# Kernel optimization log

Measured on AMD Instinct MI355X. Metric: run time of the kernel, lower is better.

## Reference

```python
import jax, jax.numpy as jnp
import numpy as np

N = 768           # atoms
C = 128           # channels (layer_dims = [128]*4)
A = 8             # atom types
RBF = 4
RBF_LOW, RBF_HIGH = 0.0, 2.5
EPS = 1e-12

# Levi-Civita tensor for the 1x1->1 tensor product
_E = np.zeros((3, 3, 3), np.float32)
_E[0, 1, 2] = _E[1, 2, 0] = _E[2, 0, 1] = 1.0
_E[0, 2, 1] = _E[2, 1, 0] = _E[1, 0, 2] = -1.0
EIJK = jnp.asarray(_E)


def setup_inputs() -> dict:
    key = jax.random.key(0)
    ks = jax.random.split(key, 16)
    r = jax.random.normal(ks[0], (N, 3), jnp.float32) * 2.0
    one_hot = jax.nn.one_hot(jax.random.randint(ks[1], (N,), 0, A), A, dtype=jnp.float32)

    def W(k, shape, fan_in):
        return jax.random.normal(k, shape, jnp.float32) / np.sqrt(fan_in).astype(np.float32)

    return dict(
        r=r, one_hot=one_hot,
        embed_W=W(ks[2], (C, A), A), embed_b=jnp.zeros((C,), jnp.float32),
        # 12 radial nets: layer0 uses ids 0-1, layer1 ids 2-6, layer2 ids 7-11
        Rw1=W(ks[3], (12, RBF, C), RBF), Rb1=jnp.zeros((12, C), jnp.float32),
        Rw2=W(ks[4], (12, C, C), C), Rb2=jnp.zeros((12, C), jnp.float32),
        si0_w0=W(ks[5], (C, C), C), si0_b0=jnp.zeros((C,), jnp.float32),
        si0_w1=W(ks[6], (C, C), C),
        si1_w0=W(ks[7], (C, 2 * C), 2 * C), si1_b0=jnp.zeros((C,), jnp.float32),
        si1_w1=W(ks[8], (C, 3 * C), 3 * C),
        si2_w0=W(ks[9], (C, 2 * C), 2 * C), si2_b0=jnp.zeros((C,), jnp.float32),
        si2_w1=W(ks[10], (C, 3 * C), 3 * C),
        nl_b0=jnp.zeros((C,), jnp.float32), nl_b1=jnp.zeros((C,), jnp.float32),
        pred_W=W(ks[11], (A, C), C), pred_b=jnp.zeros((A,), jnp.float32),
    )


def _gated(x, b):
    # norm-gated equivariant nonlinearity for l=1 features [N, C, 3]
    n = jnp.sqrt(jnp.maximum(jnp.sum(x * x, -1), EPS))
    return x * (jax.nn.elu(b[None, :] + n) / n)[..., None]


def reference(r, one_hot, embed_W, embed_b, Rw1, Rb1, Rw2, Rb2,
              si0_w0, si0_b0, si0_w1, si1_w0, si1_b0, si1_w1,
              si2_w0, si2_b0, si2_w1, nl_b0, nl_b1, pred_W, pred_b):
    rij = r[:, None, :] - r[None, :, :]                     # [N,N,3]
    dij = jnp.sqrt(jnp.maximum(jnp.sum(rij * rij, -1), EPS))  # [N,N]
    u = rij / (dij[..., None] + 1e-8)                        # unit vectors
    centers = jnp.linspace(RBF_LOW, RBF_HIGH, RBF)
    gamma = RBF / (RBF_HIGH - RBF_LOW)                       # 1 / spacing
    rbf = jnp.exp(-gamma * jnp.square(dij[..., None] - centers))  # [N,N,RBF]

    def radial(i):  # per-filter radial net on rbf features -> [N,N,C]
        h = jax.nn.relu(jnp.einsum('abr,rc->abc', rbf, Rw1[i]) + Rb1[i])
        return jnp.einsum('abc,cd->abd', h, Rw2[i]) + Rb2[i]

    def si(x, w, b=None):  # self-interaction linear over channel dim f
        y = jnp.einsum('afm,gf->agm', x, w)
        return y if b is None else y + b[:, None]

    e = (one_hot @ embed_W.T + embed_b)[..., None]           # [N,C,1]

    # layer 0: only an l=0 input exists
    c00 = jnp.einsum('abf,bfm->afm', radial(0), e)                 # 0x0->0
    c01 = jnp.einsum('abf,abi,bf->afi', radial(1), u, e[..., 0])   # 0x1->1
    x0 = jax.nn.elu(si(c00, si0_w0, si0_b0))
    x1 = _gated(si(c01, si0_w1), nl_b0)

    def full_layer(x0, x1, ri, w0, b0, w1):
        a0 = jnp.einsum('abf,bfm->afm', radial(ri), x0)                        # 0x0->0
        b1 = jnp.einsum('abf,abi,bf->afi', radial(ri + 1), u, x0[..., 0])      # 0x1->1
        a1 = jnp.einsum('abf,bfm->afm', radial(ri + 2), x1)                    # 1x0->1
        o0 = jnp.einsum('abf,abj,bfj->af', radial(ri + 3), u, x1)[..., None]   # 1x1->0
        o1 = jnp.einsum('ijk,abf,abj,bfk->afi', EIJK, radial(ri + 4), u, x1)   # 1x1->1
        y0 = si(jnp.concatenate([a0, o0], 1), w0, b0)   # [N,2C,1] -> [N,C,1]
        y1 = si(jnp.concatenate([b1, a1, o1], 1), w1)   # [N,3C,3] -> [N,C,3]
        return y0, y1

    x0, x1 = full_layer(x0, x1, 2, si1_w0, si1_b0, si1_w1)
    x0, x1 = jax.nn.elu(x0), _gated(x1, nl_b1)
    x0, x1 = full_layer(x0, x1, 7, si2_w0, si2_b0, si2_w1)  # last layer: no nonlinearity

    atom = (x0[..., 0] @ pred_W.T + pred_b)[..., None]      # [N,A,1]
    # (probability_scalars, missing_coordinates, atom_type_scalars)
    return x0, x1, atom
```

## Files before the change

### kernel.cpp

```cpp
#include <hip/hip_runtime.h>
#include <hip/hip_fp16.h>
#include <math.h>


constexpr int   N_    = 768;
constexpr int   C_    = 128;
constexpr int   M_    = 320;
constexpr float DMAX_ = 6.4f;
constexpr float GAMMA_ = 1.6f;

__global__ __launch_bounds__(256) void build_table_kernel(
    const float* __restrict__ Rw1, const float* __restrict__ Rb1,
    const float* __restrict__ Rw2, const float* __restrict__ Rb2,
    __half2* __restrict__ tab, float delta)
{
    const int f  = threadIdx.x & 127, fh = threadIdx.x >> 7;
    const int m0 = blockIdx.x * 4;

    __shared__ float hs[2][5][C_];

    float rbf[5][4];
    const float cent[4] = {0.0f, 2.5f / 3.0f, 5.0f / 3.0f, 2.5f};
#pragma unroll
    for (int mm = 0; mm < 5; ++mm) {
        int m = m0 + mm; if (m > M_ - 1) m = M_ - 1;
        const float d = (float)m * delta;
#pragma unroll
        for (int k = 0; k < 4; ++k) {
            const float t = d - cent[k];
            rbf[mm][k] = expf(-GAMMA_ * t * t);
        }
    }

    for (int ii = 0; ii < 6; ++ii) {
        const int i = fh * 6 + ii;
        float w1v[4];
#pragma unroll
        for (int k = 0; k < 4; ++k) w1v[k] = Rw1[(i * 4 + k) * C_ + f];
        const float b1v = Rb1[i * C_ + f];

        __syncthreads();
#pragma unroll
        for (int mm = 0; mm < 5; ++mm) {
            float acc = b1v;
#pragma unroll
            for (int k = 0; k < 4; ++k) acc = fmaf(rbf[mm][k], w1v[k], acc);
            hs[fh][mm][f] = fmaxf(acc, 0.0f);
        }
        __syncthreads();

        const float b2v = Rb2[i * C_ + f];
        float out[5] = {b2v, b2v, b2v, b2v, b2v};
        for (int c = 0; c < C_; ++c) {
            const float w = Rw2[(i * C_ + c) * C_ + f];
#pragma unroll
            for (int mm = 0; mm < 5; ++mm) out[mm] = fmaf(hs[fh][mm][c], w, out[mm]);
        }
#pragma unroll
        for (int mm = 0; mm < 4; ++mm) {
            const int m = m0 + mm;
            if (m < M_)
                tab[((size_t)m * 12 + i) * C_ + f] =
                    __floats2half2_rn(out[mm], out[mm + 1] - out[mm]);
        }
    }
}

__global__ __launch_bounds__(256) void embed_kernel(
    const float* __restrict__ onehot, const float* __restrict__ eW,
    const float* __restrict__ eb, float* __restrict__ e)
{
    const int idx = blockIdx.x * 256 + threadIdx.x;
    const int b = idx >> 7, f = idx & 127;
    float acc = eb[f];
#pragma unroll
    for (int t = 0; t < 8; ++t) acc = fmaf(onehot[b * 8 + t], eW[f * 8 + t], acc);
    e[idx] = acc;
}

template <int RI>
__device__ inline void pair_setup(const float* __restrict__ r, int a, int bbase,
                                  int tid, float4* pair, int* qoff)
{
    const float rax = r[a * 3 + 0], ray = r[a * 3 + 1], raz = r[a * 3 + 2];
    for (int i = tid; i < 384; i += 256) {
        const int b = bbase + i;
        const float dx = rax - r[b * 3 + 0];
        const float dy = ray - r[b * 3 + 1];
        const float dz = raz - r[b * 3 + 2];
        const float d2 = fmaf(dx, dx, fmaf(dy, dy, dz * dz));
        const float d  = sqrtf(fmaxf(d2, 1e-12f));
        const float inv = 1.0f / (d + 1e-8f);
        const float t = d * ((float)(M_ - 1) / DMAX_);
        int q = (int)t; q = q > M_ - 2 ? M_ - 2 : q;
        const float fr = fminf(t - (float)q, 1.0f);
        pair[i] = make_float4(dx * inv, dy * inv, dz * inv, fr);
        qoff[i] = (q * 12 + RI) * C_;
    }
}

__global__ __launch_bounds__(256, 8) void pair0_kernel(
    const float* __restrict__ r, const float* __restrict__ e,
    const __half2* __restrict__ tab, float* __restrict__ P)
{
    const int a = blockIdx.x >> 1, p = blockIdx.x & 1;
    const int tid = threadIdx.x;
    const int f = tid & 127, part = tid >> 7;
    const int bbase = p * 384;

    __shared__ float4 pair[384];
    __shared__ int    qoff[384];
    __shared__ float  sred[4][2][C_];

    pair_setup<0>(r, a, bbase, tid, pair, qoff);
    __syncthreads();

    float c00 = 0.f, cx = 0.f, cy = 0.f, cz = 0.f;
    const __half2* tabf = tab + f;
    const int iBeg = part * 192, iEnd = iBeg + 192;
    for (int i = iBeg; i < iEnd; ++i) {
        const float4 pr = pair[i];
        const __half2* tp = tabf + qoff[i];
        const __half2 h0 = tp[0], h1 = tp[C_];
        const float eb_ = e[(bbase + i) * C_ + f];
        const float fr = pr.w;
        const float2 v0 = __half22float2(h0);
        const float2 v1 = __half22float2(h1);
        const float t0 = fmaf(fr, v0.y, v0.x);
        const float t1 = fmaf(fr, v1.y, v1.x);
        c00 = fmaf(t0, eb_, c00);
        const float te = t1 * eb_;
        cx = fmaf(te, pr.x, cx); cy = fmaf(te, pr.y, cy); cz = fmaf(te, pr.z, cz);
    }

    sred[0][part][f] = c00;
    sred[1][part][f] = cx;
    sred[2][part][f] = cy;
    sred[3][part][f] = cz;
    __syncthreads();

    for (int idx = tid; idx < 4 * C_; idx += 256) {
        const int k = idx >> 7, c = idx & 127;
        P[((size_t)(p * N_ + a) * 4 + k) * C_ + c] =
            sred[k][0][c] + sred[k][1][c];
    }
}

template <int RI>
__global__ __launch_bounds__(256, 8) void pairF_kernel(
    const float* __restrict__ r, const uint2* __restrict__ xin,
    const __half2* __restrict__ tab, float* __restrict__ P)
{
    const int a = blockIdx.x >> 1, p = blockIdx.x & 1;
    const int tid = threadIdx.x;
    const int f = tid & 127, part = tid >> 7;
    const int bbase = p * 384;

    __shared__ float4 pair[384];
    __shared__ int    qoff[384];
    __shared__ float  sred[11][2][C_];

    pair_setup<RI>(r, a, bbase, tid, pair, qoff);
    __syncthreads();

    float a0 = 0.f, b1x = 0.f, b1y = 0.f, b1z = 0.f;
    float a1x = 0.f, a1y = 0.f, a1z = 0.f;
    float o0 = 0.f, o1x = 0.f, o1y = 0.f, o1z = 0.f;

    const __half2* tabf = tab + f;
    const uint2*   xf   = xin + (size_t)bbase * C_ + f;
    const int iBeg = part * 192, iEnd = iBeg + 192;
    for (int i = iBeg; i < iEnd; ++i) {
        const float4 pr = pair[i];
        const __half2* tp = tabf + qoff[i];
        const __half2 h0 = tp[0 * C_], h1 = tp[1 * C_], h2 = tp[2 * C_];
        const __half2 h3 = tp[3 * C_], h4 = tp[4 * C_];
        const uint2 xw = xf[(size_t)i * C_];

        const float fr = pr.w;
        const float2 v0 = __half22float2(h0);
        const float2 v1 = __half22float2(h1);
        const float2 v2 = __half22float2(h2);
        const float2 v3 = __half22float2(h3);
        const float2 v4 = __half22float2(h4);
        const float t0 = fmaf(fr, v0.y, v0.x);
        const float t1 = fmaf(fr, v1.y, v1.x);
        const float t2 = fmaf(fr, v2.y, v2.x);
        const float t3 = fmaf(fr, v3.y, v3.x);
        const float t4 = fmaf(fr, v4.y, v4.x);

        const float2 x01 = __half22float2(*(const __half2*)&xw.x);
        const float2 x23 = __half22float2(*(const __half2*)&xw.y);
        const float x0b = x01.x, xbx = x01.y, xby = x23.x, xbz = x23.y;

        a0 = fmaf(t0, x0b, a0);
        const float tb = t1 * x0b;
        b1x = fmaf(tb, pr.x, b1x); b1y = fmaf(tb, pr.y, b1y); b1z = fmaf(tb, pr.z, b1z);
        a1x = fmaf(t2, xbx, a1x); a1y = fmaf(t2, xby, a1y); a1z = fmaf(t2, xbz, a1z);
        const float ud = fmaf(pr.x, xbx, fmaf(pr.y, xby, pr.z * xbz));
        o0 = fmaf(t3, ud, o0);
        const float crx = pr.y * xbz - pr.z * xby;
        const float cry = pr.z * xbx - pr.x * xbz;
        const float crz = pr.x * xby - pr.y * xbx;
        o1x = fmaf(t4, crx, o1x); o1y = fmaf(t4, cry, o1y); o1z = fmaf(t4, crz, o1z);
    }

    sred[0][part][f] = a0;
    sred[1][part][f] = b1x; sred[2][part][f] = b1y; sred[3][part][f] = b1z;
    sred[4][part][f] = a1x; sred[5][part][f] = a1y; sred[6][part][f] = a1z;
    sred[7][part][f] = o0;
    sred[8][part][f] = o1x; sred[9][part][f] = o1y; sred[10][part][f] = o1z;
    __syncthreads();

    for (int idx = tid; idx < 11 * C_; idx += 256) {
        const int k = idx >> 7, c = idx & 127;
        P[((size_t)(p * N_ + a) * 11 + k) * C_ + c] =
            sred[k][0][c] + sred[k][1][c];
    }
}

__global__ __launch_bounds__(512) void finish0_kernel(
    const float* __restrict__ P,
    const float* __restrict__ w0, const float* __restrict__ b0v,
    const float* __restrict__ w1, const float* __restrict__ nlb,
    uint2* __restrict__ xout)
{
    const int a = blockIdx.x, tid = threadIdx.x;
    const int f = tid & 127;

    __shared__ float s[4 * C_];
    __shared__ float ys[4 * C_];

    for (int idx = tid; idx < 4 * C_; idx += 512)
        s[idx] = P[(size_t)a * 4 * C_ + idx] +
                 P[((size_t)(N_ + a) * 4) * C_ + idx];
    __syncthreads();

    {
        const int j = tid >> 7;
        float y;
        if (j == 0) {
            y = b0v[f];
            const float4* w = (const float4*)(w0 + (size_t)f * C_);
            for (int c4 = 0; c4 < C_ / 4; ++c4) {
                const float4 wv = w[c4];
                y = fmaf(wv.x, s[c4 * 4 + 0], y);
                y = fmaf(wv.y, s[c4 * 4 + 1], y);
                y = fmaf(wv.z, s[c4 * 4 + 2], y);
                y = fmaf(wv.w, s[c4 * 4 + 3], y);
            }
        } else {
            y = 0.f;
            const float4* w = (const float4*)(w1 + (size_t)f * C_);
            const float* sj = s + j * C_;
            for (int c4 = 0; c4 < C_ / 4; ++c4) {
                const float4 wv = w[c4];
                y = fmaf(wv.x, sj[c4 * 4 + 0], y);
                y = fmaf(wv.y, sj[c4 * 4 + 1], y);
                y = fmaf(wv.z, sj[c4 * 4 + 2], y);
                y = fmaf(wv.w, sj[c4 * 4 + 3], y);
            }
        }
        ys[j * C_ + f] = y;
    }
    __syncthreads();

    if (tid < C_) {
        const float y0 = ys[tid];
        const float yx = ys[C_ + tid], yy = ys[2 * C_ + tid], yz = ys[3 * C_ + tid];
        const float x0v = y0 > 0.f ? y0 : expm1f(y0);
        const float nsq = fmaf(yx, yx, fmaf(yy, yy, yz * yz));
        const float nn  = sqrtf(fmaxf(nsq, 1e-12f));
        const float g   = nlb[tid] + nn;
        const float sc  = (g > 0.f ? g : expm1f(g)) / nn;
        uint2 w;
        *(__half2*)&w.x = __floats2half2_rn(x0v, yx * sc);
        *(__half2*)&w.y = __floats2half2_rn(yy * sc, yz * sc);
        xout[(size_t)a * C_ + tid] = w;
    }
}

template <bool NONLIN, bool LAST>
__global__ __launch_bounds__(512) void finishF_kernel(
    const float* __restrict__ P,
    const float* __restrict__ w0, const float* __restrict__ b0v,
    const float* __restrict__ w1, const float* __restrict__ nlb,
    uint2* __restrict__ xout,
    float* __restrict__ out, const float* __restrict__ predW,
    const float* __restrict__ predb)
{
    const int a = blockIdx.x, tid = threadIdx.x;
    const int f = tid & 127;

    __shared__ float s[11 * C_];
    __shared__ float ys[4 * C_];

    for (int idx = tid; idx < 11 * C_; idx += 512)
        s[idx] = P[(size_t)a * 11 * C_ + idx] +
                 P[((size_t)(N_ + a) * 11) * C_ + idx];
    __syncthreads();

    {
        const int j = tid >> 7;
        float y;
        if (j == 0) {
            y = b0v[f];
            const float4* w = (const float4*)(w0 + (size_t)f * (2 * C_));
            const float* s0 = s + 0 * C_;
            const float* s7 = s + 7 * C_;
            for (int c4 = 0; c4 < C_ / 4; ++c4) {
                const float4 wa = w[c4];
                const float4 wb = w[C_ / 4 + c4];
                y = fmaf(wa.x, s0[c4 * 4 + 0], y);
                y = fmaf(wa.y, s0[c4 * 4 + 1], y);
                y = fmaf(wa.z, s0[c4 * 4 + 2], y);
                y = fmaf(wa.w, s0[c4 * 4 + 3], y);
                y = fmaf(wb.x, s7[c4 * 4 + 0], y);
                y = fmaf(wb.y, s7[c4 * 4 + 1], y);
                y = fmaf(wb.z, s7[c4 * 4 + 2], y);
                y = fmaf(wb.w, s7[c4 * 4 + 3], y);
            }
        } else {
            y = 0.f;
            const float4* w = (const float4*)(w1 + (size_t)f * (3 * C_));
            const float* sb = s + j * C_;
            const float* sa = s + (3 + j) * C_;
            const float* so = s + (7 + j) * C_;
            for (int c4 = 0; c4 < C_ / 4; ++c4) {
                const float4 w_b = w[c4];
                const float4 w_a = w[C_ / 4 + c4];
                const float4 w_o = w[2 * (C_ / 4) + c4];
                y = fmaf(w_b.x, sb[c4 * 4 + 0], y);
                y = fmaf(w_b.y, sb[c4 * 4 + 1], y);
                y = fmaf(w_b.z, sb[c4 * 4 + 2], y);
                y = fmaf(w_b.w, sb[c4 * 4 + 3], y);
                y = fmaf(w_a.x, sa[c4 * 4 + 0], y);
                y = fmaf(w_a.y, sa[c4 * 4 + 1], y);
                y = fmaf(w_a.z, sa[c4 * 4 + 2], y);
                y = fmaf(w_a.w, sa[c4 * 4 + 3], y);
                y = fmaf(w_o.x, so[c4 * 4 + 0], y);
                y = fmaf(w_o.y, so[c4 * 4 + 1], y);
                y = fmaf(w_o.z, so[c4 * 4 + 2], y);
                y = fmaf(w_o.w, so[c4 * 4 + 3], y);
            }
        }
        ys[j * C_ + f] = y;
    }
    __syncthreads();

    if (NONLIN) {
        if (tid < C_) {
            const float y0 = ys[tid];
            const float yx = ys[C_ + tid], yy = ys[2 * C_ + tid], yz = ys[3 * C_ + tid];
            const float x0v = y0 > 0.f ? y0 : expm1f(y0);
            const float nsq = fmaf(yx, yx, fmaf(yy, yy, yz * yz));
            const float nn  = sqrtf(fmaxf(nsq, 1e-12f));
            const float g   = nlb[tid] + nn;
            const float sc  = (g > 0.f ? g : expm1f(g)) / nn;
            uint2 w;
            *(__half2*)&w.x = __floats2half2_rn(x0v, yx * sc);
            *(__half2*)&w.y = __floats2half2_rn(yy * sc, yz * sc);
            xout[(size_t)a * C_ + tid] = w;
        }
    }
    if (LAST) {
        if (tid < C_) {
            const float y0 = ys[tid];
            const float yx = ys[C_ + tid], yy = ys[2 * C_ + tid], yz = ys[3 * C_ + tid];
            out[a * C_ + tid] = y0;
            float* o1 = out + N_ * C_;
            o1[a * (C_ * 3) + tid * 3 + 0] = yx;
            o1[a * (C_ * 3) + tid * 3 + 1] = yy;
            o1[a * (C_ * 3) + tid * 3 + 2] = yz;
        }
        __syncthreads();
        if (tid < 8) {
            float acc = predb[tid];
            for (int c = 0; c < C_; ++c)
                acc = fmaf(predW[tid * C_ + c], ys[c], acc);
            out[N_ * C_ + N_ * C_ * 3 + a * 8 + tid] = acc;
        }
    }
}

extern "C" void kernel_launch(void* const* d_in, const int* in_sizes, int n_in,
                              void* d_out, int out_size, void* d_ws, size_t ws_size,
                              hipStream_t stream)
{
    const float* r       = (const float*)d_in[0];
    const float* onehot  = (const float*)d_in[1];
    const float* embed_W = (const float*)d_in[2];
    const float* embed_b = (const float*)d_in[3];
    const float* Rw1     = (const float*)d_in[4];
    const float* Rb1     = (const float*)d_in[5];
    const float* Rw2     = (const float*)d_in[6];
    const float* Rb2     = (const float*)d_in[7];
    const float* si0_w0  = (const float*)d_in[8];
    const float* si0_b0  = (const float*)d_in[9];
    const float* si0_w1  = (const float*)d_in[10];
    const float* si1_w0  = (const float*)d_in[11];
    const float* si1_b0  = (const float*)d_in[12];
    const float* si1_w1  = (const float*)d_in[13];
    const float* si2_w0  = (const float*)d_in[14];
    const float* si2_b0  = (const float*)d_in[15];
    const float* si2_w1  = (const float*)d_in[16];
    const float* nl_b0   = (const float*)d_in[17];
    const float* nl_b1   = (const float*)d_in[18];
    const float* pred_W  = (const float*)d_in[19];
    const float* pred_b  = (const float*)d_in[20];
    (void)in_sizes; (void)n_in; (void)out_size; (void)ws_size;

    const float delta = DMAX_ / (float)(M_ - 1);

    char* wsb = (char*)d_ws;
    __half2* table = (__half2*)wsb;
    float*   e     = (float*)(wsb + 1966080);
    uint2*   xa    = (uint2*)(wsb + 1966080 + 393216);
    uint2*   xb    = (uint2*)(wsb + 1966080 + 393216 + 786432);
    float*   P     = (float*)(wsb + 1966080 + 393216 + 786432 * 2);

    float* out = (float*)d_out;

    build_table_kernel<<<M_ / 4, 256, 0, stream>>>(Rw1, Rb1, Rw2, Rb2, table, delta);
    embed_kernel<<<(N_ * C_) / 256, 256, 0, stream>>>(onehot, embed_W, embed_b, e);

    pair0_kernel<<<2 * N_, 256, 0, stream>>>(r, e, table, P);
    finish0_kernel<<<N_, 512, 0, stream>>>(P, si0_w0, si0_b0, si0_w1, nl_b0, xa);

    pairF_kernel<2><<<2 * N_, 256, 0, stream>>>(r, xa, table, P);
    finishF_kernel<true, false><<<N_, 512, 0, stream>>>(
        P, si1_w0, si1_b0, si1_w1, nl_b1, xb, nullptr, nullptr, nullptr);

    pairF_kernel<7><<<2 * N_, 256, 0, stream>>>(r, xb, table, P);
    finishF_kernel<false, true><<<N_, 512, 0, stream>>>(
        P, si2_w0, si2_b0, si2_w1, nullptr, nullptr, out, pred_W, pred_b);
}
```

Measured before the change: 537.5 us.

## Split pair work three ways, batch atoms in finish kernels, enlarge radial table

The pair kernels now split each atom's neighbours into three chunks instead of two, which launches more, smaller blocks and gives better occupancy. The finish kernels each handle three atoms per block, so every weight load is reused across three atoms, and they sum three partial buffers. The radial lookup table grows from 320 to 512 entries, which makes it more accurate but larger in cache. The RI template parameter becomes a runtime argument, and the half-to-float conversions are rewritten. The extra partial sums add global traffic in the finish stage, and the fewer finish blocks (256) may leave the GPU underfilled.

```diff
diff --git a/kernel.cpp b/kernel.cpp
--- a/kernel.cpp
+++ b/kernel.cpp
@@ -3,11 +3,18 @@
 #include <math.h>
 
 
-constexpr int   N_    = 768;
-constexpr int   C_    = 128;
-constexpr int   M_    = 320;
-constexpr float DMAX_ = 6.4f;
+constexpr int   N_     = 768;
+constexpr int   C_     = 128;
+constexpr int   M_     = 512;
+constexpr int   NSPLIT = 3;
+constexpr int   NB_    = N_ / NSPLIT;
+constexpr int   TA_    = 3;
+constexpr float DMAX_  = 6.4f;
 constexpr float GAMMA_ = 1.6f;
+
+__device__ inline float lerp_vd(float fr, __half2 vd) {
+    return fmaf(fr, __half2float(__high2half(vd)), __half2float(__low2half(vd)));
+}
 
 __global__ __launch_bounds__(256) void build_table_kernel(
     const float* __restrict__ Rw1, const float* __restrict__ Rb1,
@@ -78,12 +85,11 @@
     e[idx] = acc;
 }
 
-template <int RI>
 __device__ inline void pair_setup(const float* __restrict__ r, int a, int bbase,
-                                  int tid, float4* pair, int* qoff)
+                                  int tid, int RI, float4* pair, int* qoff)
 {
     const float rax = r[a * 3 + 0], ray = r[a * 3 + 1], raz = r[a * 3 + 2];
-    for (int i = tid; i < 384; i += 256) {
+    for (int i = tid; i < NB_; i += 256) {
         const int b = bbase + i;
         const float dx = rax - r[b * 3 + 0];
         const float dy = ray - r[b * 3 + 1];
@@ -103,31 +109,30 @@
     const float* __restrict__ r, const float* __restrict__ e,
     const __half2* __restrict__ tab, float* __restrict__ P)
 {
-    const int a = blockIdx.x >> 1, p = blockIdx.x & 1;
+    const int a = blockIdx.x / NSPLIT, p = blockIdx.x - a * NSPLIT;
     const int tid = threadIdx.x;
     const int f = tid & 127, part = tid >> 7;
-    const int bbase = p * 384;
-
-    __shared__ float4 pair[384];
-    __shared__ int    qoff[384];
+    const int bbase = p * NB_;
+
+    __shared__ float4 pair[NB_];
+    __shared__ int    qoff[NB_];
     __shared__ float  sred[4][2][C_];
 
-    pair_setup<0>(r, a, bbase, tid, pair, qoff);
+    pair_setup(r, a, bbase, tid, 0, pair, qoff);
     __syncthreads();
 
     float c00 = 0.f, cx = 0.f, cy = 0.f, cz = 0.f;
     const __half2* tabf = tab + f;
-    const int iBeg = part * 192, iEnd = iBeg + 192;
+    const float*   ef   = e + (size_t)bbase * C_ + f;
+    const int iBeg = part * (NB_ / 2), iEnd = iBeg + (NB_ / 2);
     for (int i = iBeg; i < iEnd; ++i) {
         const float4 pr = pair[i];
         const __half2* tp = tabf + qoff[i];
         const __half2 h0 = tp[0], h1 = tp[C_];
-        const float eb_ = e[(bbase + i) * C_ + f];
+        const float eb_ = ef[(size_t)i * C_];
         const float fr = pr.w;
-        const float2 v0 = __half22float2(h0);
-        const float2 v1 = __half22float2(h1);
-        const float t0 = fmaf(fr, v0.y, v0.x);
-        const float t1 = fmaf(fr, v1.y, v1.x);
+        const float t0 = lerp_vd(fr, h0);
+        const float t1 = lerp_vd(fr, h1);
         c00 = fmaf(t0, eb_, c00);
         const float te = t1 * eb_;
         cx = fmaf(te, pr.x, cx); cy = fmaf(te, pr.y, cy); cz = fmaf(te, pr.z, cz);
@@ -141,26 +146,24 @@
 
     for (int idx = tid; idx < 4 * C_; idx += 256) {
         const int k = idx >> 7, c = idx & 127;
-        P[((size_t)(p * N_ + a) * 4 + k) * C_ + c] =
-            sred[k][0][c] + sred[k][1][c];
-    }
-}
-
-template <int RI>
+        P[((size_t)(p * N_ + a) * 4) * C_ + idx] = sred[k][0][c] + sred[k][1][c];
+    }
+}
+
 __global__ __launch_bounds__(256, 8) void pairF_kernel(
     const float* __restrict__ r, const uint2* __restrict__ xin,
-    const __half2* __restrict__ tab, float* __restrict__ P)
-{
-    const int a = blockIdx.x >> 1, p = blockIdx.x & 1;
+    const __half2* __restrict__ tab, int RI, float* __restrict__ P)
+{
+    const int a = blockIdx.x / NSPLIT, p = blockIdx.x - a * NSPLIT;
     const int tid = threadIdx.x;
     const int f = tid & 127, part = tid >> 7;
-    const int bbase = p * 384;
-
-    __shared__ float4 pair[384];
-    __shared__ int    qoff[384];
+    const int bbase = p * NB_;
+
+    __shared__ float4 pair[NB_];
+    __shared__ int    qoff[NB_];
     __shared__ float  sred[11][2][C_];
 
-    pair_setup<RI>(r, a, bbase, tid, pair, qoff);
+    pair_setup(r, a, bbase, tid, RI, pair, qoff);
     __syncthreads();
 
     float a0 = 0.f, b1x = 0.f, b1y = 0.f, b1z = 0.f;
@@ -169,7 +172,7 @@
 
     const __half2* tabf = tab + f;
     const uint2*   xf   = xin + (size_t)bbase * C_ + f;
-    const int iBeg = part * 192, iEnd = iBeg + 192;
+    const int iBeg = part * (NB_ / 2), iEnd = iBeg + (NB_ / 2);
     for (int i = iBeg; i < iEnd; ++i) {
         const float4 pr = pair[i];
         const __half2* tp = tabf + qoff[i];
@@ -178,20 +181,18 @@
         const uint2 xw = xf[(size_t)i * C_];
 
         const float fr = pr.w;
-        const float2 v0 = __half22float2(h0);
-        const float2 v1 = __half22float2(h1);
-        const float2 v2 = __half22float2(h2);
-        const float2 v3 = __half22float2(h3);
-        const float2 v4 = __half22float2(h4);
-        const float t0 = fmaf(fr, v0.y, v0.x);
-        const float t1 = fmaf(fr, v1.y, v1.x);
-        const float t2 = fmaf(fr, v2.y, v2.x);
-        const float t3 = fmaf(fr, v3.y, v3.x);
-        const float t4 = fmaf(fr, v4.y, v4.x);
-
-        const float2 x01 = __half22float2(*(const __half2*)&xw.x);
-        const float2 x23 = __half22float2(*(const __half2*)&xw.y);
-        const float x0b = x01.x, xbx = x01.y, xby = x23.x, xbz = x23.y;
+        const float t0 = lerp_vd(fr, h0);
+        const float t1 = lerp_vd(fr, h1);
+        const float t2 = lerp_vd(fr, h2);
+        const float t3 = lerp_vd(fr, h3);
+        const float t4 = lerp_vd(fr, h4);
+
+        const __half2 xh01 = *(const __half2*)&xw.x;
+        const __half2 xh23 = *(const __half2*)&xw.y;
+        const float x0b = __half2float(__low2half(xh01));
+        const float xbx = __half2float(__high2half(xh01));
+        const float xby = __half2float(__low2half(xh23));
+        const float xbz = __half2float(__high2half(xh23));
 
         a0 = fmaf(t0, x0b, a0);
         const float tb = t1 * x0b;
@@ -214,8 +215,7 @@
 
     for (int idx = tid; idx < 11 * C_; idx += 256) {
         const int k = idx >> 7, c = idx & 127;
-        P[((size_t)(p * N_ + a) * 11 + k) * C_ + c] =
-            sred[k][0][c] + sred[k][1][c];
+        P[((size_t)(p * N_ + a) * 11) * C_ + idx] = sred[k][0][c] + sred[k][1][c];
     }
 }
 
@@ -225,58 +225,71 @@
     const float* __restrict__ w1, const float* __restrict__ nlb,
     uint2* __restrict__ xout)
 {
-    const int a = blockIdx.x, tid = threadIdx.x;
-    const int f = tid & 127;
-
-    __shared__ float s[4 * C_];
-    __shared__ float ys[4 * C_];
-
-    for (int idx = tid; idx < 4 * C_; idx += 512)
-        s[idx] = P[(size_t)a * 4 * C_ + idx] +
-                 P[((size_t)(N_ + a) * 4) * C_ + idx];
-    __syncthreads();
-
-    {
-        const int j = tid >> 7;
-        float y;
-        if (j == 0) {
-            y = b0v[f];
-            const float4* w = (const float4*)(w0 + (size_t)f * C_);
-            for (int c4 = 0; c4 < C_ / 4; ++c4) {
-                const float4 wv = w[c4];
-                y = fmaf(wv.x, s[c4 * 4 + 0], y);
-                y = fmaf(wv.y, s[c4 * 4 + 1], y);
-                y = fmaf(wv.z, s[c4 * 4 + 2], y);
-                y = fmaf(wv.w, s[c4 * 4 + 3], y);
+    const int a0_ = blockIdx.x * TA_, tid = threadIdx.x;
+    const int f = tid & 127, j = tid >> 7;
+
+    __shared__ float s[TA_][4 * C_];
+    __shared__ float ys[TA_][4 * C_];
+
+    for (int t = 0; t < TA_; ++t)
+        for (int idx = tid; idx < 4 * C_; idx += 512) {
+            float acc = 0.f;
+            for (int sp = 0; sp < NSPLIT; ++sp)
+                acc += P[((size_t)(sp * N_ + a0_ + t) * 4) * C_ + idx];
+            s[t][idx] = acc;
+        }
+    __syncthreads();
+
+    float acc[TA_];
+    if (j == 0) {
+        const float b0 = b0v[f];
+#pragma unroll
+        for (int t = 0; t < TA_; ++t) acc[t] = b0;
+        const float4* w = (const float4*)(w0 + (size_t)f * C_);
+        for (int c4 = 0; c4 < C_ / 4; ++c4) {
+            const float4 wv = w[c4];
+#pragma unroll
+            for (int t = 0; t < TA_; ++t) {
+                const float4 sv = *(const float4*)&s[t][c4 * 4];
+                acc[t] = fmaf(wv.x, sv.x, acc[t]);
+                acc[t] = fmaf(wv.y, sv.y, acc[t]);
+                acc[t] = fmaf(wv.z, sv.z, acc[t]);
+                acc[t] = fmaf(wv.w, sv.w, acc[t]);
             }
-        } else {
-            y = 0.f;
-            const float4* w = (const float4*)(w1 + (size_t)f * C_);
-            const float* sj = s + j * C_;
-            for (int c4 = 0; c4 < C_ / 4; ++c4) {
-                const float4 wv = w[c4];
-                y = fmaf(wv.x, sj[c4 * 4 + 0], y);
-                y = fmaf(wv.y, sj[c4 * 4 + 1], y);
-                y = fmaf(wv.z, sj[c4 * 4 + 2], y);
-                y = fmaf(wv.w, sj[c4 * 4 + 3], y);
+        }
+    } else {
+#pragma unroll
+        for (int t = 0; t < TA_; ++t) acc[t] = 0.f;
+        const float4* w = (const float4*)(w1 + (size_t)f * C_);
+        for (int c4 = 0; c4 < C_ / 4; ++c4) {
+            const float4 wv = w[c4];
+#pragma unroll
+            for (int t = 0; t < TA_; ++t) {
+                const float4 sv = *(const float4*)&s[t][j * C_ + c4 * 4];
+                acc[t] = fmaf(wv.x, sv.x, acc[t]);
+                acc[t] = fmaf(wv.y, sv.y, acc[t]);
+                acc[t] = fmaf(wv.z, sv.z, acc[t]);
+                acc[t] = fmaf(wv.w, sv.w, acc[t]);
             }
         }
-        ys[j * C_ + f] = y;
-    }
-    __syncthreads();
-
-    if (tid < C_) {
-        const float y0 = ys[tid];
-        const float yx = ys[C_ + tid], yy = ys[2 * C_ + tid], yz = ys[3 * C_ + tid];
+    }
+#pragma unroll
+    for (int t = 0; t < TA_; ++t) ys[t][j * C_ + f] = acc[t];
+    __syncthreads();
+
+    if (tid < TA_ * C_) {
+        const int t = tid >> 7, ff = tid & 127;
+        const float y0 = ys[t][ff];
+        const float yx = ys[t][C_ + ff], yy = ys[t][2 * C_ + ff], yz = ys[t][3 * C_ + ff];
         const float x0v = y0 > 0.f ? y0 : expm1f(y0);
         const float nsq = fmaf(yx, yx, fmaf(yy, yy, yz * yz));
         const float nn  = sqrtf(fmaxf(nsq, 1e-12f));
-        const float g   = nlb[tid] + nn;
+        const float g   = nlb[ff] + nn;
         const float sc  = (g > 0.f ? g : expm1f(g)) / nn;
         uint2 w;
         *(__half2*)&w.x = __floats2half2_rn(x0v, yx * sc);
         *(__half2*)&w.y = __floats2half2_rn(yy * sc, yz * sc);
-        xout[(size_t)a * C_ + tid] = w;
+        xout[(size_t)(a0_ + t) * C_ + ff] = w;
     }
 }
 
@@ -289,96 +302,110 @@
     float* __restrict__ out, const float* __restrict__ predW,
     const float* __restrict__ predb)
 {
-    const int a = blockIdx.x, tid = threadIdx.x;
-    const int f = tid & 127;
-
-    __shared__ float s[11 * C_];
-    __shared__ float ys[4 * C_];
-
-    for (int idx = tid; idx < 11 * C_; idx += 512)
-        s[idx] = P[(size_t)a * 11 * C_ + idx] +
-                 P[((size_t)(N_ + a) * 11) * C_ + idx];
-    __syncthreads();
-
-    {
-        const int j = tid >> 7;
-        float y;
-        if (j == 0) {
-            y = b0v[f];
-            const float4* w = (const float4*)(w0 + (size_t)f * (2 * C_));
-            const float* s0 = s + 0 * C_;
-            const float* s7 = s + 7 * C_;
-            for (int c4 = 0; c4 < C_ / 4; ++c4) {
-                const float4 wa = w[c4];
-                const float4 wb = w[C_ / 4 + c4];
-                y = fmaf(wa.x, s0[c4 * 4 + 0], y);
-                y = fmaf(wa.y, s0[c4 * 4 + 1], y);
-                y = fmaf(wa.z, s0[c4 * 4 + 2], y);
-                y = fmaf(wa.w, s0[c4 * 4 + 3], y);
-                y = fmaf(wb.x, s7[c4 * 4 + 0], y);
-                y = fmaf(wb.y, s7[c4 * 4 + 1], y);
-                y = fmaf(wb.z, s7[c4 * 4 + 2], y);
-                y = fmaf(wb.w, s7[c4 * 4 + 3], y);
+    const int a0_ = blockIdx.x * TA_, tid = threadIdx.x;
+    const int f = tid & 127, j = tid >> 7;
+
+    __shared__ float s[TA_][11 * C_];
+    __shared__ float ys[TA_][4 * C_];
+
+    for (int t = 0; t < TA_; ++t)
+        for (int idx = tid; idx < 11 * C_; idx += 512) {
+            float acc = 0.f;
+            for (int sp = 0; sp < NSPLIT; ++sp)
+                acc += P[((size_t)(sp * N_ + a0_ + t) * 11) * C_ + idx];
+            s[t][idx] = acc;
+        }
+    __syncthreads();
+
+    float acc[TA_];
+    if (j == 0) {
+        const float b0 = b0v[f];
+#pragma unroll
+        for (int t = 0; t < TA_; ++t) acc[t] = b0;
+        const float4* w = (const float4*)(w0 + (size_t)f * (2 * C_));
+        for (int c4 = 0; c4 < C_ / 4; ++c4) {
+            const float4 wa = w[c4];
+            const float4 wb = w[C_ / 4 + c4];
+#pragma unroll
+            for (int t = 0; t < TA_; ++t) {
+                const float4 s0 = *(const float4*)&s[t][c4 * 4];
+                const float4 s7 = *(const float4*)&s[t][7 * C_ + c4 * 4];
+                acc[t] = fmaf(wa.x, s0.x, acc[t]);
+                acc[t] = fmaf(wa.y, s0.y, acc[t]);
+                acc[t] = fmaf(wa.z, s0.z, acc[t]);
+                acc[t] = fmaf(wa.w, s0.w, acc[t]);
+                acc[t] = fmaf(wb.x, s7.x, acc[t]);
+                acc[t] = fmaf(wb.y, s7.y, acc[t]);
+                acc[t] = fmaf(wb.z, s7.z, acc[t]);
+                acc[t] = fmaf(wb.w, s7.w, acc[t]);
             }
-        } else {
-            y = 0.f;
-            const float4* w = (const float4*)(w1 + (size_t)f * (3 * C_));
-            const float* sb = s + j * C_;
-            const float* sa = s + (3 + j) * C_;
-            const float* so = s + (7 + j) * C_;
-            for (int c4 = 0; c4 < C_ / 4; ++c4) {
-                const float4 w_b = w[c4];
-                const float4 w_a = w[C_ / 4 + c4];
-                const float4 w_o = w[2 * (C_ / 4) + c4];
-                y = fmaf(w_b.x, sb[c4 * 4 + 0], y);
-                y = fmaf(w_b.y, sb[c4 * 4 + 1], y);
-                y = fmaf(w_b.z, sb[c4 * 4 + 2], y);
-                y = fmaf(w_b.w, sb[c4 * 4 + 3], y);
-                y = fmaf(w_a.x, sa[c4 * 4 + 0], y);
-                y = fmaf(w_a.y, sa[c4 * 4 + 1], y);
-                y = fmaf(w_a.z, sa[c4 * 4 + 2], y);
-                y = fmaf(w_a.w, sa[c4 * 4 + 3], y);
-                y = fmaf(w_o.x, so[c4 * 4 + 0], y);
-                y = fmaf(w_o.y, so[c4 * 4 + 1], y);
-                y = fmaf(w_o.z, so[c4 * 4 + 2], y);
-                y = fmaf(w_o.w, so[c4 * 4 + 3], y);
+        }
+    } else {
+#pragma unroll
+        for (int t = 0; t < TA_; ++t) acc[t] = 0.f;
+        const float4* w = (const float4*)(w1 + (size_t)f * (3 * C_));
+        for (int c4 = 0; c4 < C_ / 4; ++c4) {
+            const float4 wb = w[c4];
+            const float4 wa = w[C_ / 4 + c4];
+            const float4 wo = w[2 * (C_ / 4) + c4];
+#pragma unroll
+            for (int t = 0; t < TA_; ++t) {
+                const float4 sb = *(const float4*)&s[t][j * C_ + c4 * 4];
+                const float4 sa = *(const float4*)&s[t][(3 + j) * C_ + c4 * 4];
+                const float4 so = *(const float4*)&s[t][(7 + j) * C_ + c4 * 4];
+                acc[t] = fmaf(wb.x, sb.x, acc[t]);
+                acc[t] = fmaf(wb.y, sb.y, acc[t]);
+                acc[t] = fmaf(wb.z, sb.z, acc[t]);
+                acc[t] = fmaf(wb.w, sb.w, acc[t]);
+                acc[t] = fmaf(wa.x, sa.x, acc[t]);
+                acc[t] = fmaf(wa.y, sa.y, acc[t]);
+                acc[t] = fmaf(wa.z, sa.z, acc[t]);
+                acc[t] = fmaf(wa.w, sa.w, acc[t]);
+                acc[t] = fmaf(wo.x, so.x, acc[t]);
+                acc[t] = fmaf(wo.y, so.y, acc[t]);
+                acc[t] = fmaf(wo.z, so.z, acc[t]);
+                acc[t] = fmaf(wo.w, so.w, acc[t]);
             }
         }
-        ys[j * C_ + f] = y;
-    }
+    }
+#pragma unroll
+    for (int t = 0; t < TA_; ++t) ys[t][j * C_ + f] = acc[t];
     __syncthreads();
 
     if (NONLIN) {
-        if (tid < C_) {
-            const float y0 = ys[tid];
-            const float yx = ys[C_ + tid], yy = ys[2 * C_ + tid], yz = ys[3 * C_ + tid];
+        if (tid < TA_ * C_) {
+            const int t = tid >> 7, ff = tid & 127;
+            const float y0 = ys[t][ff];
+            const float yx = ys[t][C_ + ff], yy = ys[t][2 * C_ + ff], yz = ys[t][3 * C_ + ff];
             const float x0v = y0 > 0.f ? y0 : expm1f(y0);
             const float nsq = fmaf(yx, yx, fmaf(yy, yy, yz * yz));
             const float nn  = sqrtf(fmaxf(nsq, 1e-12f));
-            const float g   = nlb[tid] + nn;
+            const float g   = nlb[ff] + nn;
             const float sc  = (g > 0.f ? g : expm1f(g)) / nn;
             uint2 w;
             *(__half2*)&w.x = __floats2half2_rn(x0v, yx * sc);
             *(__half2*)&w.y = __floats2half2_rn(yy * sc, yz * sc);
-            xout[(size_t)a * C_ + tid] = w;
+            xout[(size_t)(a0_ + t) * C_ + ff] = w;
         }
     }
     if (LAST) {
-        if (tid < C_) {
-            const float y0 = ys[tid];
-            const float yx = ys[C_ + tid], yy = ys[2 * C_ + tid], yz = ys[3 * C_ + tid];
-            out[a * C_ + tid] = y0;
+        if (tid < TA_ * C_) {
+            const int t = tid >> 7, ff = tid & 127;
+            const int a = a0_ + t;
+            const float y0 = ys[t][ff];
+            const float yx = ys[t][C_ + ff], yy = ys[t][2 * C_ + ff], yz = ys[t][3 * C_ + ff];
+            out[a * C_ + ff] = y0;
             float* o1 = out + N_ * C_;
-            o1[a * (C_ * 3) + tid * 3 + 0] = yx;
-            o1[a * (C_ * 3) + tid * 3 + 1] = yy;
-            o1[a * (C_ * 3) + tid * 3 + 2] = yz;
-        }
-        __syncthreads();
-        if (tid < 8) {
-            float acc = predb[tid];
+            o1[a * (C_ * 3) + ff * 3 + 0] = yx;
+            o1[a * (C_ * 3) + ff * 3 + 1] = yy;
+            o1[a * (C_ * 3) + ff * 3 + 2] = yz;
+        }
+        if (tid < TA_ * 8) {
+            const int t = tid >> 3, o = tid & 7;
+            float acc2 = predb[o];
             for (int c = 0; c < C_; ++c)
-                acc = fmaf(predW[tid * C_ + c], ys[c], acc);
-            out[N_ * C_ + N_ * C_ * 3 + a * 8 + tid] = acc;
+                acc2 = fmaf(predW[o * C_ + c], ys[t][c], acc2);
+            out[N_ * C_ + N_ * C_ * 3 + (a0_ + t) * 8 + o] = acc2;
         }
     }
 }
@@ -413,25 +440,26 @@
     const float delta = DMAX_ / (float)(M_ - 1);
 
     char* wsb = (char*)d_ws;
-    __half2* table = (__half2*)wsb;
-    float*   e     = (float*)(wsb + 1966080);
-    uint2*   xa    = (uint2*)(wsb + 1966080 + 393216);
-    uint2*   xb    = (uint2*)(wsb + 1966080 + 393216 + 786432);
-    float*   P     = (float*)(wsb + 1966080 + 393216 + 786432 * 2);
+    size_t off = 0;
+    __half2* table = (__half2*)(wsb + off); off += (size_t)M_ * 12 * C_ * 4;
+    float*   e     = (float*)(wsb + off);   off += (size_t)N_ * C_ * 4;
+    uint2*   xa    = (uint2*)(wsb + off);   off += (size_t)N_ * C_ * 8;
+    uint2*   xb    = (uint2*)(wsb + off);   off += (size_t)N_ * C_ * 8;
+    float*   P     = (float*)(wsb + off);
 
     float* out = (float*)d_out;
 
     build_table_kernel<<<M_ / 4, 256, 0, stream>>>(Rw1, Rb1, Rw2, Rb2, table, delta);
     embed_kernel<<<(N_ * C_) / 256, 256, 0, stream>>>(onehot, embed_W, embed_b, e);
 
-    pair0_kernel<<<2 * N_, 256, 0, stream>>>(r, e, table, P);
-    finish0_kernel<<<N_, 512, 0, stream>>>(P, si0_w0, si0_b0, si0_w1, nl_b0, xa);
-
-    pairF_kernel<2><<<2 * N_, 256, 0, stream>>>(r, xa, table, P);
-    finishF_kernel<true, false><<<N_, 512, 0, stream>>>(
+    pair0_kernel<<<NSPLIT * N_, 256, 0, stream>>>(r, e, table, P);
+    finish0_kernel<<<N_ / TA_, 512, 0, stream>>>(P, si0_w0, si0_b0, si0_w1,
+                                                 nl_b0, xa);
+    pairF_kernel<<<NSPLIT * N_, 256, 0, stream>>>(r, xa, table, 2, P);
+    finishF_kernel<true, false><<<N_ / TA_, 512, 0, stream>>>(
         P, si1_w0, si1_b0, si1_w1, nl_b1, xb, nullptr, nullptr, nullptr);
 
-    pairF_kernel<7><<<2 * N_, 256, 0, stream>>>(r, xb, table, P);
-    finishF_kernel<false, true><<<N_, 512, 0, stream>>>(
+    pairF_kernel<<<NSPLIT * N_, 256, 0, stream>>>(r, xb, table, 7, P);
+    finishF_kernel<false, true><<<N_ / TA_, 512, 0, stream>>>(
         P, si2_w0, si2_b0, si2_w1, nullptr, nullptr, out, pred_W, pred_b);
 }
```

Result: faster. 496.5 us (-7.6%).
